# Kernel tuning notes

Measured on AMD Instinct MI355X. Metric: run time of the kernel, lower is better.

The kernel has to match this reference:

```python
import jax, jax.numpy as jnp
import numpy as np

B, NQ, C = 2, 10000, 256
M, L, K = 8, 3, 4
D = C // M
LEVEL_SHAPES = [(100, 100), (50, 50), (25, 25)]


def setup_inputs() -> dict:
    key = jax.random.key(0)
    ks = jax.random.split(key, 16)
    inp = {
        "query": jax.random.normal(ks[0], (B, NQ, C), jnp.float32),
        "reference_points": jax.random.uniform(ks[1], (B, NQ, 2), jnp.float32),
        "value0": jax.random.normal(ks[2], (B, C) + LEVEL_SHAPES[0], jnp.float32),
        "value1": jax.random.normal(ks[3], (B, C) + LEVEL_SHAPES[1], jnp.float32),
        "value2": jax.random.normal(ks[4], (B, C) + LEVEL_SHAPES[2], jnp.float32),
        "Wv": jax.random.normal(ks[5], (C, C), jnp.float32) * 0.02,
        "bv": jnp.zeros((C,), jnp.float32),
        "Ws": jax.random.normal(ks[6], (M * L * K * 2, C), jnp.float32) * 0.05,
        "bs": jax.random.normal(ks[7], (M * L * K * 2,), jnp.float32),
        "Wa": jax.random.normal(ks[8], (M * L * K, C), jnp.float32) * 0.02,
        "ba": jnp.zeros((M * L * K,), jnp.float32),
        "Wo": jax.random.normal(ks[9], (C, C), jnp.float32) * 0.02,
        "bo": jnp.zeros((C,), jnp.float32),
    }
    return inp


def _bilinear_sample(vflat, px, py, H, W):
    """grid_sample bilinear, align_corners=False, padding_mode='zeros'.
    vflat: (B, M, H*W, D); px, py: (B, M, Q, K) pixel coords. -> (B, M, Q, K, D)
    """
    b, m, q, k = px.shape
    x0 = jnp.floor(px)
    y0 = jnp.floor(py)
    wx1 = px - x0  # frac weights (grad 1 w.r.t. px, matching grid_sample)
    wy1 = py - y0
    wx0 = 1.0 - wx1
    wy0 = 1.0 - wy1

    def gather(xi, yi):
        valid = ((xi >= 0) & (xi <= W - 1) & (yi >= 0) & (yi <= H - 1)).astype(vflat.dtype)
        xc = jnp.clip(xi, 0, W - 1).astype(jnp.int32)
        yc = jnp.clip(yi, 0, H - 1).astype(jnp.int32)
        idx = (yc * W + xc).reshape(b, m, q * k)
        g = jnp.take_along_axis(vflat, idx[..., None], axis=2)  # (B,M,QK,D)
        return g.reshape(b, m, q, k, -1) * valid[..., None]

    out = (gather(x0, y0) * (wx0 * wy0)[..., None]
           + gather(x0 + 1, y0) * (wx1 * wy0)[..., None]
           + gather(x0, y0 + 1) * (wx0 * wy1)[..., None]
           + gather(x0 + 1, y0 + 1) * (wx1 * wy1)[..., None])
    return out


def reference(query, reference_points, value0, value1, value2,
              Wv, bv, Ws, bs, Wa, ba, Wo, bo):
    bsz, nq, c = query.shape
    dt = query.dtype
    # sampling offsets and attention weights
    off = (query @ Ws.T + bs).reshape(bsz, nq, M, L, K, 2)
    attn = jax.nn.softmax((query @ Wa.T + ba).reshape(bsz, nq, M, L * K), axis=-1)
    attn = attn.reshape(bsz, nq, M, L, K)

    out = jnp.zeros((bsz, nq, M, D), dt)
    for li, v in enumerate([value0, value1, value2]):
        H, W = v.shape[2], v.shape[3]
        # conv1x1 value projection -> per-head maps (B, M, H*W, D)
        proj = jnp.einsum('bchw,oc->bohw', v, Wv) + bv[None, :, None, None]
        vflat = proj.reshape(bsz, M, D, H * W).transpose(0, 1, 3, 2)
        norm = jnp.asarray([W, H], dt)
        loc = reference_points[:, :, None, None, :] + off[:, :, :, li, :, :] / norm  # (B,Q,M,K,2)
        # grid = loc*2-1; pixel = (grid+1)*size/2 - 0.5 = loc*size - 0.5
        px = (loc[..., 0] * W - 0.5).transpose(0, 2, 1, 3)  # (B,M,Q,K)
        py = (loc[..., 1] * H - 0.5).transpose(0, 2, 1, 3)
        sampled = _bilinear_sample(vflat, px, py, H, W)  # (B,M,Q,K,D)
        out = out + jnp.einsum('bmqkd,bqmk->bqmd', sampled, attn[:, :, :, li, :])

    out = out.reshape(bsz, nq, c)
    return out @ Wo.T + bo
```

## Files before the change

### kernel.cpp

```cpp
#include <hip/hip_runtime.h>
#include <cstddef>

#define B_ 2
#define NQ_ 10000
#define C_ 256
#define M_ 8
#define L_ 3
#define K_ 4
#define D_ 32
#define P_ 13125

typedef unsigned short u16;
typedef __attribute__((ext_vector_type(8))) short short8;
typedef __attribute__((ext_vector_type(4))) float f32x4;

static __device__ __forceinline__ u16 f2bf(float f) {
    union { float f; unsigned u; } x; x.f = f;
    unsigned r = x.u + 0x7fffu + ((x.u >> 16) & 1u);
    return (u16)(r >> 16);
}
static __device__ __forceinline__ short8 cvt8(const float4& a, const float4& b) {
    short8 r;
    r[0] = (short)f2bf(a.x); r[1] = (short)f2bf(a.y);
    r[2] = (short)f2bf(a.z); r[3] = (short)f2bf(a.w);
    r[4] = (short)f2bf(b.x); r[5] = (short)f2bf(b.y);
    r[6] = (short)f2bf(b.z); r[7] = (short)f2bf(b.w);
    return r;
}

__global__ __launch_bounds__(256) void prep(
    const float* __restrict__ v0, const float* __restrict__ v1,
    const float* __restrict__ v2, u16* __restrict__ Vt,
    const float* __restrict__ Wv, const float* __restrict__ Ws,
    const float* __restrict__ Wa, const float* __restrict__ Wo,
    u16* __restrict__ wb,
    const float* __restrict__ query, u16* __restrict__ qbf)
{
    __shared__ u16 tile[64][66];
    const int bid = blockIdx.x;
    const int t   = threadIdx.x;

    if (bid < 3768) {
        constexpr int HWs[3]  = {10000, 2500, 625};
        constexpr int offs[3] = {0, 10000, 12500};
        const int x = bid % 157;
        const int y = (bid / 157) % 4;
        const int z = bid / 628;
        const int b   = z / 3;
        const int lvl = z % 3;
        const int HW  = HWs[lvl];
        const int p0  = x * 64;
        if (p0 >= HW) return;
        const int c0  = y * 64;

        const float* V = (lvl == 0 ? v0 : (lvl == 1 ? v1 : v2)) + (size_t)b * 256 * HW;

        const int pl = t & 63;
        const int cb = t >> 6;
        #pragma unroll
        for (int i = 0; i < 16; ++i) {
            int c = cb + i * 4;
            float vv = 0.f;
            if (p0 + pl < HW)
                vv = V[(size_t)(c0 + c) * HW + p0 + pl];
            tile[pl][c] = f2bf(vv);
        }
        __syncthreads();

        const int cl = t & 63;
        const int pb = t >> 6;
        #pragma unroll
        for (int i = 0; i < 16; ++i) {
            int p = pb + i * 4;
            if (p0 + p < HW)
                Vt[((size_t)b * P_ + offs[lvl] + p0 + p) * 256 + c0 + cl] = tile[p][cl];
        }
    } else if (bid < 3868) {
        const int i = (bid - 3768) * 256 + t;
        if (i >= 25600) return;
        const int g = i * 8;
        const float* src;
        if (g < 65536)       src = Wv + g;
        else if (g < 114688) src = Ws + (g - 65536);
        else if (g < 139264) src = Wa + (g - 114688);
        else                 src = Wo + (g - 139264);
        const float4 a = *reinterpret_cast<const float4*>(src);
        const float4 b = *reinterpret_cast<const float4*>(src + 4);
        *reinterpret_cast<short8*>(wb + g) = cvt8(a, b);
    } else {
        const int i = (bid - 3868) * 256 + t;
        const float4 a = *reinterpret_cast<const float4*>(query + (size_t)i * 8);
        const float4 b = *reinterpret_cast<const float4*>(query + (size_t)i * 8 + 4);
        *reinterpret_cast<short8*>(qbf + (size_t)i * 8) = cvt8(a, b);
    }
}

__global__ __launch_bounds__(512) void gemm_fused(
    const u16* __restrict__ Vt, const u16* __restrict__ qbf,
    const u16* __restrict__ Wvb, const float* __restrict__ bv,
    const u16* __restrict__ Wsb, const float* __restrict__ bs,
    const u16* __restrict__ Wab, const float* __restrict__ ba,
    u16* __restrict__ proj, float* __restrict__ S)
{
    __shared__ u16 Bs[64 * 264];

    const bool jobS = (blockIdx.x >= 416);
    const int  bid  = jobS ? (blockIdx.x - 416) : blockIdx.x;

    const int npanel    = jobS ? 5 : 4;
    const int nRowTiles = jobS ? 79 : 103;
    const int rows      = jobS ? (B_ * NQ_) : (B_ * P_);
    const int N1        = jobS ? 192 : 256;
    const int Ntot      = jobS ? 288 : 256;
    const u16* Aimg     = jobS ? qbf : Vt;
    const u16* B1b      = jobS ? Wsb : Wvb;
    const u16* B2b      = jobS ? Wab : Wvb;
    const float* bias1  = jobS ? bs : bv;
    const float* bias2  = jobS ? ba : bv;

    const int rlo  = bid & 7;
    const int tmp  = bid >> 3;
    const int panel = tmp % npanel;
    const int rowTile = (tmp / npanel) * 8 + rlo;
    if (rowTile >= nRowTiles) return;

    const int t  = threadIdx.x;
    const int w  = t >> 6;
    const int l  = t & 63;
    const int row0 = rowTile * 256 + w * 32;
    const int o0   = panel * 64;
    const int lr = l & 15;
    const int kb = (l >> 4) * 8;

    const int ra0 = min(row0 + lr,      rows - 1);
    const int ra1 = min(row0 + 16 + lr, rows - 1);
    const u16* Ap0 = Aimg + (size_t)ra0 * 256 + kb;
    const u16* Ap1 = Aimg + (size_t)ra1 * 256 + kb;

    short8 A0[4], A1[4];
    #pragma unroll
    for (int i = 0; i < 4; ++i) {
        A0[i] = *reinterpret_cast<const short8*>(Ap0 + i * 32);
        A1[i] = *reinterpret_cast<const short8*>(Ap1 + i * 32);
    }

    #pragma unroll
    for (int i = 0; i < 4; ++i) {
        int idx = i * 512 + t;
        int col = idx >> 5;
        int kc  = (idx & 31) * 8;
        int colg = min(o0 + col, Ntot - 1);
        const u16* Br = ((colg < N1) ? B1b + (size_t)colg * 256
                                     : B2b + (size_t)(colg - N1) * 256) + kc;
        *reinterpret_cast<short8*>(&Bs[col * 264 + kc]) =
            *reinterpret_cast<const short8*>(Br);
    }

    __syncthreads();

    short8 A0b[4], A1b[4];
    #pragma unroll
    for (int i = 0; i < 4; ++i) {
        A0b[i] = *reinterpret_cast<const short8*>(Ap0 + 128 + i * 32);
        A1b[i] = *reinterpret_cast<const short8*>(Ap1 + 128 + i * 32);
    }

    f32x4 acc[2][4] = {};
    #pragma unroll
    for (int i = 0; i < 8; ++i) {
        const int k0 = i * 32;
        short8 a0 = (i < 4) ? A0[i] : A0b[i - 4];
        short8 a1 = (i < 4) ? A1[i] : A1b[i - 4];
        short8 b0 = *reinterpret_cast<const short8*>(&Bs[(0 * 16 + lr) * 264 + kb + k0]);
        short8 b1 = *reinterpret_cast<const short8*>(&Bs[(1 * 16 + lr) * 264 + kb + k0]);
        short8 b2 = *reinterpret_cast<const short8*>(&Bs[(2 * 16 + lr) * 264 + kb + k0]);
        short8 b3 = *reinterpret_cast<const short8*>(&Bs[(3 * 16 + lr) * 264 + kb + k0]);
        acc[0][0] = __builtin_amdgcn_mfma_f32_16x16x32_bf16(a0, b0, acc[0][0], 0, 0, 0);
        acc[0][1] = __builtin_amdgcn_mfma_f32_16x16x32_bf16(a0, b1, acc[0][1], 0, 0, 0);
        acc[0][2] = __builtin_amdgcn_mfma_f32_16x16x32_bf16(a0, b2, acc[0][2], 0, 0, 0);
        acc[0][3] = __builtin_amdgcn_mfma_f32_16x16x32_bf16(a0, b3, acc[0][3], 0, 0, 0);
        acc[1][0] = __builtin_amdgcn_mfma_f32_16x16x32_bf16(a1, b0, acc[1][0], 0, 0, 0);
        acc[1][1] = __builtin_amdgcn_mfma_f32_16x16x32_bf16(a1, b1, acc[1][1], 0, 0, 0);
        acc[1][2] = __builtin_amdgcn_mfma_f32_16x16x32_bf16(a1, b2, acc[1][2], 0, 0, 0);
        acc[1][3] = __builtin_amdgcn_mfma_f32_16x16x32_bf16(a1, b3, acc[1][3], 0, 0, 0);
    }

    const int orow = (l >> 4) * 4;

    if (jobS) {
        #pragma unroll
        for (int ct = 0; ct < 4; ++ct) {
            const int col = o0 + ct * 16 + lr;
            if (col >= Ntot) continue;
            const float bsv = (col < N1) ? bias1[col] : bias2[col - N1];
            #pragma unroll
            for (int rt = 0; rt < 2; ++rt) {
                #pragma unroll
                for (int r = 0; r < 4; ++r) {
                    const int row = row0 + rt * 16 + orow + r;
                    if (row < rows)
                        S[(size_t)row * 288 + col] = acc[rt][ct][r] + bsv;
                }
            }
        }
    } else {
        __syncthreads();
        #pragma unroll
        for (int ct = 0; ct < 4; ++ct) {
            const int col = ct * 16 + lr;
            const float bsv = bias1[o0 + col];
            #pragma unroll
            for (int rt = 0; rt < 2; ++rt) {
                #pragma unroll
                for (int r = 0; r < 4; ++r) {
                    const int rowL = w * 32 + rt * 16 + orow + r;
                    Bs[rowL * 64 + col] = f2bf(acc[rt][ct][r] + bsv);
                }
            }
        }
        __syncthreads();
        const int rowL = t >> 1;
        const int half = (t & 1) * 32;
        const int grow = rowTile * 256 + rowL;
        if (grow < rows) {
            const short8* src = reinterpret_cast<const short8*>(&Bs[rowL * 64 + half]);
            short8* dst = reinterpret_cast<short8*>(proj + (size_t)grow * 256 + o0 + half);
            dst[0] = src[0]; dst[1] = src[1];
            dst[2] = src[2]; dst[3] = src[3];
        }
    }
}

__global__ __launch_bounds__(512) void gemm_out(
    const u16* __restrict__ Av, int rows, int nRowTiles, int npanel,
    const u16* __restrict__ Bb, const float* __restrict__ bias, int Ntot,
    float* __restrict__ Cout)
{
    __shared__ u16 Bs[64 * 264];

    const int bid  = blockIdx.x;
    const int rlo  = bid & 7;
    const int tmp  = bid >> 3;
    const int panel = tmp % npanel;
    const int rowTile = (tmp / npanel) * 8 + rlo;
    if (rowTile >= nRowTiles) return;

    const int t  = threadIdx.x;
    const int w  = t >> 6;
    const int l  = t & 63;
    const int row0 = rowTile * 256 + w * 32;
    const int o0   = panel * 64;
    const int lr = l & 15;
    const int kb = (l >> 4) * 8;

    const int ra0 = min(row0 + lr,      rows - 1);
    const int ra1 = min(row0 + 16 + lr, rows - 1);
    const u16* Ap0 = Av + (size_t)ra0 * 256 + kb;
    const u16* Ap1 = Av + (size_t)ra1 * 256 + kb;

    short8 A0[4], A1[4];
    #pragma unroll
    for (int i = 0; i < 4; ++i) {
        A0[i] = *reinterpret_cast<const short8*>(Ap0 + i * 32);
        A1[i] = *reinterpret_cast<const short8*>(Ap1 + i * 32);
    }

    #pragma unroll
    for (int i = 0; i < 4; ++i) {
        int idx = i * 512 + t;
        int col = idx >> 5;
        int kc  = (idx & 31) * 8;
        int colg = min(o0 + col, Ntot - 1);
        *reinterpret_cast<short8*>(&Bs[col * 264 + kc]) =
            *reinterpret_cast<const short8*>(Bb + (size_t)colg * 256 + kc);
    }

    __syncthreads();

    short8 A0b[4], A1b[4];
    #pragma unroll
    for (int i = 0; i < 4; ++i) {
        A0b[i] = *reinterpret_cast<const short8*>(Ap0 + 128 + i * 32);
        A1b[i] = *reinterpret_cast<const short8*>(Ap1 + 128 + i * 32);
    }

    f32x4 acc[2][4] = {};
    #pragma unroll
    for (int i = 0; i < 8; ++i) {
        const int k0 = i * 32;
        short8 a0 = (i < 4) ? A0[i] : A0b[i - 4];
        short8 a1 = (i < 4) ? A1[i] : A1b[i - 4];
        short8 b0 = *reinterpret_cast<const short8*>(&Bs[(0 * 16 + lr) * 264 + kb + k0]);
        short8 b1 = *reinterpret_cast<const short8*>(&Bs[(1 * 16 + lr) * 264 + kb + k0]);
        short8 b2 = *reinterpret_cast<const short8*>(&Bs[(2 * 16 + lr) * 264 + kb + k0]);
        short8 b3 = *reinterpret_cast<const short8*>(&Bs[(3 * 16 + lr) * 264 + kb + k0]);
        acc[0][0] = __builtin_amdgcn_mfma_f32_16x16x32_bf16(a0, b0, acc[0][0], 0, 0, 0);
        acc[0][1] = __builtin_amdgcn_mfma_f32_16x16x32_bf16(a0, b1, acc[0][1], 0, 0, 0);
        acc[0][2] = __builtin_amdgcn_mfma_f32_16x16x32_bf16(a0, b2, acc[0][2], 0, 0, 0);
        acc[0][3] = __builtin_amdgcn_mfma_f32_16x16x32_bf16(a0, b3, acc[0][3], 0, 0, 0);
        acc[1][0] = __builtin_amdgcn_mfma_f32_16x16x32_bf16(a1, b0, acc[1][0], 0, 0, 0);
        acc[1][1] = __builtin_amdgcn_mfma_f32_16x16x32_bf16(a1, b1, acc[1][1], 0, 0, 0);
        acc[1][2] = __builtin_amdgcn_mfma_f32_16x16x32_bf16(a1, b2, acc[1][2], 0, 0, 0);
        acc[1][3] = __builtin_amdgcn_mfma_f32_16x16x32_bf16(a1, b3, acc[1][3], 0, 0, 0);
    }

    const int orow = (l >> 4) * 4;
    #pragma unroll
    for (int ct = 0; ct < 4; ++ct) {
        const int col = o0 + ct * 16 + lr;
        if (col >= Ntot) continue;
        const float bsv = bias[col];
        #pragma unroll
        for (int rt = 0; rt < 2; ++rt) {
            #pragma unroll
            for (int r = 0; r < 4; ++r) {
                const int row = row0 + rt * 16 + orow + r;
                if (row < rows)
                    Cout[(size_t)row * Ntot + col] = acc[rt][ct][r] + bsv;
            }
        }
    }
}

__global__ __launch_bounds__(256) void sample_kernel(
    const float* __restrict__ S,
    const float* __restrict__ refp,
    const u16* __restrict__ proj,
    u16* __restrict__ out2)
{
    constexpr int Wd[3]   = {100, 50, 25};
    constexpr int offs[3] = {0, 10000, 12500};

    __shared__ int   midx[192][4];
    __shared__ float mw[192][4];

    const int t = threadIdx.x;

    if (t < 192) {
        const int q  = t / 96;
        const int tq = t % 96;
        const int tm = tq / 12;
        const int tj = tq % 12;
        const int bq = blockIdx.x * 2 + q;
        const float* Sq = S + (size_t)bq * 288;

        float lg[12], mx = -1e30f;
        #pragma unroll
        for (int jj = 0; jj < 12; ++jj) {
            lg[jj] = Sq[192 + tm * 12 + jj];
            mx = fmaxf(mx, lg[jj]);
        }
        float sum = 0.f;
        #pragma unroll
        for (int jj = 0; jj < 12; ++jj) sum += __expf(lg[jj] - mx);
        const float attn = __expf(lg[tj] - mx) / sum;

        const int l  = tj >> 2;
        const int Wl = Wd[l];
        const float refx = refp[(size_t)bq * 2 + 0];
        const float refy = refp[(size_t)bq * 2 + 1];
        const float ox = Sq[(tm * 12 + tj) * 2 + 0];
        const float oy = Sq[(tm * 12 + tj) * 2 + 1];
        const float px = refx * (float)Wl + ox - 0.5f;
        const float py = refy * (float)Wl + oy - 0.5f;
        const float x0f = floorf(px), y0f = floorf(py);
        const float wx1 = px - x0f, wy1 = py - y0f;
        const float wx0 = 1.f - wx1, wy0 = 1.f - wy1;
        const int x0 = (int)x0f, y0 = (int)y0f;
        const int x1 = x0 + 1, y1 = y0 + 1;
        const bool vx0 = (unsigned)x0 < (unsigned)Wl;
        const bool vx1 = (unsigned)x1 < (unsigned)Wl;
        const bool vy0 = (unsigned)y0 < (unsigned)Wl;
        const bool vy1 = (unsigned)y1 < (unsigned)Wl;
        const int chb  = tm * 32;
        const int base = offs[l];
        midx[t][0] = (vx0 && vy0) ? ((base + y0 * Wl + x0) * 256 + chb) : 0;
        midx[t][1] = (vx1 && vy0) ? ((base + y0 * Wl + x1) * 256 + chb) : 0;
        midx[t][2] = (vx0 && vy1) ? ((base + y1 * Wl + x0) * 256 + chb) : 0;
        midx[t][3] = (vx1 && vy1) ? ((base + y1 * Wl + x1) * 256 + chb) : 0;
        mw[t][0] = (vx0 && vy0) ? attn * wx0 * wy0 : 0.f;
        mw[t][1] = (vx1 && vy0) ? attn * wx1 * wy0 : 0.f;
        mw[t][2] = (vx0 && vy1) ? attn * wx0 * wy1 : 0.f;
        mw[t][3] = (vx1 && vy1) ? attn * wx1 * wy1 : 0.f;
    }
    __syncthreads();

    const int qi  = t >> 7;
    const int tt  = t & 127;
    const int mh  = tt >> 4;
    const int d16 = tt & 15;
    const int bq2 = blockIdx.x * 2 + qi;
    const int b   = bq2 / NQ_;
    const u16* projb = proj + (size_t)b * P_ * 256 + 2 * d16;

    float acc0 = 0.f, acc1 = 0.f;

    #pragma unroll
    for (int j = 0; j < 12; ++j) {
        const int mj = qi * 96 + mh * 12 + j;
        const int4   o  = *reinterpret_cast<const int4*>(midx[mj]);
        const float4 ww = *reinterpret_cast<const float4*>(mw[mj]);
        const unsigned u00 = *reinterpret_cast<const unsigned*>(projb + o.x);
        const unsigned u10 = *reinterpret_cast<const unsigned*>(projb + o.y);
        const unsigned u01 = *reinterpret_cast<const unsigned*>(projb + o.z);
        const unsigned u11 = *reinterpret_cast<const unsigned*>(projb + o.w);
        union { unsigned u; float f; } c0, c1;
        c0.u = u00 << 16;          c1.u = u00 & 0xffff0000u;
        acc0 = fmaf(ww.x, c0.f, acc0); acc1 = fmaf(ww.x, c1.f, acc1);
        c0.u = u10 << 16;          c1.u = u10 & 0xffff0000u;
        acc0 = fmaf(ww.y, c0.f, acc0); acc1 = fmaf(ww.y, c1.f, acc1);
        c0.u = u01 << 16;          c1.u = u01 & 0xffff0000u;
        acc0 = fmaf(ww.z, c0.f, acc0); acc1 = fmaf(ww.z, c1.f, acc1);
        c0.u = u11 << 16;          c1.u = u11 & 0xffff0000u;
        acc0 = fmaf(ww.w, c0.f, acc0); acc1 = fmaf(ww.w, c1.f, acc1);
    }

    const unsigned packed = (unsigned)f2bf(acc0) | ((unsigned)f2bf(acc1) << 16);
    *reinterpret_cast<unsigned*>(out2 + (size_t)bq2 * 256 + mh * 32 + 2 * d16) = packed;
}

extern "C" void kernel_launch(void* const* d_in, const int* in_sizes, int n_in,
                              void* d_out, int out_size, void* d_ws, size_t ws_size,
                              hipStream_t stream)
{
    const float* query = (const float*)d_in[0];
    const float* refp  = (const float*)d_in[1];
    const float* v0    = (const float*)d_in[2];
    const float* v1    = (const float*)d_in[3];
    const float* v2    = (const float*)d_in[4];
    const float* Wv    = (const float*)d_in[5];
    const float* bv    = (const float*)d_in[6];
    const float* Ws    = (const float*)d_in[7];
    const float* bs    = (const float*)d_in[8];
    const float* Wa    = (const float*)d_in[9];
    const float* ba    = (const float*)d_in[10];
    const float* Wo    = (const float*)d_in[11];
    const float* bo    = (const float*)d_in[12];
    float* out = (float*)d_out;

    char* wsb = (char*)d_ws;
    u16*   proj  = (u16*)wsb;    wsb += (size_t)B_ * P_ * 256 * 2;
    float* S     = (float*)wsb;  wsb += (size_t)B_ * NQ_ * 288 * 4;
    u16*   Vt    = (u16*)wsb;    wsb += (size_t)B_ * P_ * 256 * 2;
    u16*   out2  = (u16*)wsb;    wsb += (size_t)B_ * NQ_ * 256 * 2;
    u16*   qbf   = (u16*)wsb;    wsb += (size_t)B_ * NQ_ * 256 * 2;
    u16*   wb    = (u16*)wsb;    wsb += (size_t)204800 * 2;
    u16* Wvb = wb;
    u16* Wsb = wb + 65536;
    u16* Wab = wb + 114688;
    u16* Wob = wb + 139264;

    prep<<<dim3(6368), dim3(256), 0, stream>>>(
        v0, v1, v2, Vt, Wv, Ws, Wa, Wo, wb, query, qbf);

    gemm_fused<<<dim3(816), dim3(512), 0, stream>>>(
        Vt, qbf, Wvb, bv, Wsb, bs, Wab, ba, proj, S);

    sample_kernel<<<dim3(NQ_), dim3(256), 0, stream>>>(S, refp, proj, out2);

    gemm_out<<<dim3(320), dim3(512), 0, stream>>>(
        out2, B_ * NQ_, 79, 4, Wob, bo, 256, out);
}
```

Measured before the change: 193.1 us.

## Reschedule kernels so value transpose overlaps the offset/attention GEMM

Splits the old prep kernel into a small weight/query bf16 conversion kernel. The value-map transpose moves into a combined kernel with the query-side offset/attention GEMM, so the two independent jobs share one launch. The value projection GEMM becomes its own kernel that runs after the transpose. This adds a fifth launch and an extra dependency step, in exchange for better packing of independent work across CUs.

```diff
diff --git a/kernel.cpp b/kernel.cpp
--- a/kernel.cpp
+++ b/kernel.cpp
@@ -28,55 +28,16 @@
     return r;
 }
 
-__global__ __launch_bounds__(256) void prep(
-    const float* __restrict__ v0, const float* __restrict__ v1,
-    const float* __restrict__ v2, u16* __restrict__ Vt,
+__global__ __launch_bounds__(256) void cvt_wq(
     const float* __restrict__ Wv, const float* __restrict__ Ws,
     const float* __restrict__ Wa, const float* __restrict__ Wo,
     u16* __restrict__ wb,
     const float* __restrict__ query, u16* __restrict__ qbf)
 {
-    __shared__ u16 tile[64][66];
     const int bid = blockIdx.x;
     const int t   = threadIdx.x;
-
-    if (bid < 3768) {
-        constexpr int HWs[3]  = {10000, 2500, 625};
-        constexpr int offs[3] = {0, 10000, 12500};
-        const int x = bid % 157;
-        const int y = (bid / 157) % 4;
-        const int z = bid / 628;
-        const int b   = z / 3;
-        const int lvl = z % 3;
-        const int HW  = HWs[lvl];
-        const int p0  = x * 64;
-        if (p0 >= HW) return;
-        const int c0  = y * 64;
-
-        const float* V = (lvl == 0 ? v0 : (lvl == 1 ? v1 : v2)) + (size_t)b * 256 * HW;
-
-        const int pl = t & 63;
-        const int cb = t >> 6;
-        #pragma unroll
-        for (int i = 0; i < 16; ++i) {
-            int c = cb + i * 4;
-            float vv = 0.f;
-            if (p0 + pl < HW)
-                vv = V[(size_t)(c0 + c) * HW + p0 + pl];
-            tile[pl][c] = f2bf(vv);
-        }
-        __syncthreads();
-
-        const int cl = t & 63;
-        const int pb = t >> 6;
-        #pragma unroll
-        for (int i = 0; i < 16; ++i) {
-            int p = pb + i * 4;
-            if (p0 + p < HW)
-                Vt[((size_t)b * P_ + offs[lvl] + p0 + p) * 256 + c0 + cl] = tile[p][cl];
-        }
-    } else if (bid < 3868) {
-        const int i = (bid - 3768) * 256 + t;
+    if (bid < 100) {
+        const int i = bid * 256 + t;
         if (i >= 25600) return;
         const int g = i * 8;
         const float* src;
@@ -88,41 +49,169 @@
         const float4 b = *reinterpret_cast<const float4*>(src + 4);
         *reinterpret_cast<short8*>(wb + g) = cvt8(a, b);
     } else {
-        const int i = (bid - 3868) * 256 + t;
+        const int i = (bid - 100) * 256 + t;
         const float4 a = *reinterpret_cast<const float4*>(query + (size_t)i * 8);
         const float4 b = *reinterpret_cast<const float4*>(query + (size_t)i * 8 + 4);
         *reinterpret_cast<short8*>(qbf + (size_t)i * 8) = cvt8(a, b);
     }
 }
 
-__global__ __launch_bounds__(512) void gemm_fused(
-    const u16* __restrict__ Vt, const u16* __restrict__ qbf,
-    const u16* __restrict__ Wvb, const float* __restrict__ bv,
+__global__ __launch_bounds__(512) void trans_s(
+    const float* __restrict__ v0, const float* __restrict__ v1,
+    const float* __restrict__ v2, u16* __restrict__ Vt,
+    const u16* __restrict__ qbf,
     const u16* __restrict__ Wsb, const float* __restrict__ bs,
     const u16* __restrict__ Wab, const float* __restrict__ ba,
-    u16* __restrict__ proj, float* __restrict__ S)
+    float* __restrict__ S)
 {
     __shared__ u16 Bs[64 * 264];
-
-    const bool jobS = (blockIdx.x >= 416);
-    const int  bid  = jobS ? (blockIdx.x - 416) : blockIdx.x;
-
-    const int npanel    = jobS ? 5 : 4;
-    const int nRowTiles = jobS ? 79 : 103;
-    const int rows      = jobS ? (B_ * NQ_) : (B_ * P_);
-    const int N1        = jobS ? 192 : 256;
-    const int Ntot      = jobS ? 288 : 256;
-    const u16* Aimg     = jobS ? qbf : Vt;
-    const u16* B1b      = jobS ? Wsb : Wvb;
-    const u16* B2b      = jobS ? Wab : Wvb;
-    const float* bias1  = jobS ? bs : bv;
-    const float* bias2  = jobS ? ba : bv;
-
+    const int t = threadIdx.x;
+
+    if (blockIdx.x < 400) {
+        const int bid = blockIdx.x;
+        const int rlo  = bid & 7;
+        const int tmp  = bid >> 3;
+        const int panel = tmp % 5;
+        const int rowTile = (tmp / 5) * 8 + rlo;
+        if (rowTile >= 79) return;
+
+        const int rows = B_ * NQ_;
+        const int N1 = 192, Ntot = 288;
+
+        const int w  = t >> 6;
+        const int l  = t & 63;
+        const int row0 = rowTile * 256 + w * 32;
+        const int o0   = panel * 64;
+        const int lr = l & 15;
+        const int kb = (l >> 4) * 8;
+
+        const int ra0 = min(row0 + lr,      rows - 1);
+        const int ra1 = min(row0 + 16 + lr, rows - 1);
+        const u16* Ap0 = qbf + (size_t)ra0 * 256 + kb;
+        const u16* Ap1 = qbf + (size_t)ra1 * 256 + kb;
+
+        short8 A0[4], A1[4];
+        #pragma unroll
+        for (int i = 0; i < 4; ++i) {
+            A0[i] = *reinterpret_cast<const short8*>(Ap0 + i * 32);
+            A1[i] = *reinterpret_cast<const short8*>(Ap1 + i * 32);
+        }
+
+        #pragma unroll
+        for (int i = 0; i < 4; ++i) {
+            int idx = i * 512 + t;
+            int col = idx >> 5;
+            int kc  = (idx & 31) * 8;
+            int colg = min(o0 + col, Ntot - 1);
+            const u16* Br = ((colg < N1) ? Wsb + (size_t)colg * 256
+                                         : Wab + (size_t)(colg - N1) * 256) + kc;
+            *reinterpret_cast<short8*>(&Bs[col * 264 + kc]) =
+                *reinterpret_cast<const short8*>(Br);
+        }
+
+        __syncthreads();
+
+        short8 A0b[4], A1b[4];
+        #pragma unroll
+        for (int i = 0; i < 4; ++i) {
+            A0b[i] = *reinterpret_cast<const short8*>(Ap0 + 128 + i * 32);
+            A1b[i] = *reinterpret_cast<const short8*>(Ap1 + 128 + i * 32);
+        }
+
+        f32x4 acc[2][4] = {};
+        #pragma unroll
+        for (int i = 0; i < 8; ++i) {
+            const int k0 = i * 32;
+            short8 a0 = (i < 4) ? A0[i] : A0b[i - 4];
+            short8 a1 = (i < 4) ? A1[i] : A1b[i - 4];
+            short8 b0 = *reinterpret_cast<const short8*>(&Bs[(0 * 16 + lr) * 264 + kb + k0]);
+            short8 b1 = *reinterpret_cast<const short8*>(&Bs[(1 * 16 + lr) * 264 + kb + k0]);
+            short8 b2 = *reinterpret_cast<const short8*>(&Bs[(2 * 16 + lr) * 264 + kb + k0]);
+            short8 b3 = *reinterpret_cast<const short8*>(&Bs[(3 * 16 + lr) * 264 + kb + k0]);
+            acc[0][0] = __builtin_amdgcn_mfma_f32_16x16x32_bf16(a0, b0, acc[0][0], 0, 0, 0);
+            acc[0][1] = __builtin_amdgcn_mfma_f32_16x16x32_bf16(a0, b1, acc[0][1], 0, 0, 0);
+            acc[0][2] = __builtin_amdgcn_mfma_f32_16x16x32_bf16(a0, b2, acc[0][2], 0, 0, 0);
+            acc[0][3] = __builtin_amdgcn_mfma_f32_16x16x32_bf16(a0, b3, acc[0][3], 0, 0, 0);
+            acc[1][0] = __builtin_amdgcn_mfma_f32_16x16x32_bf16(a1, b0, acc[1][0], 0, 0, 0);
+            acc[1][1] = __builtin_amdgcn_mfma_f32_16x16x32_bf16(a1, b1, acc[1][1], 0, 0, 0);
+            acc[1][2] = __builtin_amdgcn_mfma_f32_16x16x32_bf16(a1, b2, acc[1][2], 0, 0, 0);
+            acc[1][3] = __builtin_amdgcn_mfma_f32_16x16x32_bf16(a1, b3, acc[1][3], 0, 0, 0);
+        }
+
+        const int orow = (l >> 4) * 4;
+        #pragma unroll
+        for (int ct = 0; ct < 4; ++ct) {
+            const int col = o0 + ct * 16 + lr;
+            if (col >= Ntot) continue;
+            const float bsv = (col < N1) ? bs[col] : ba[col - N1];
+            #pragma unroll
+            for (int rt = 0; rt < 2; ++rt) {
+                #pragma unroll
+                for (int r = 0; r < 4; ++r) {
+                    const int row = row0 + rt * 16 + orow + r;
+                    if (row < rows)
+                        S[(size_t)row * 288 + col] = acc[rt][ct][r] + bsv;
+                }
+            }
+        }
+    } else {
+        constexpr int HWs[3]  = {10000, 2500, 625};
+        constexpr int offs[3] = {0, 10000, 12500};
+        const int tb = blockIdx.x - 400;
+        const int x = tb % 157;
+        const int y = (tb / 157) % 2;
+        const int z = tb / 314;
+        const int b   = z / 3;
+        const int lvl = z % 3;
+        const int HW  = HWs[lvl];
+        const int p0  = x * 64;
+        if (p0 >= HW) return;
+
+        u16 (*tile)[64][66] = reinterpret_cast<u16 (*)[64][66]>(Bs);
+        const int cc = t >> 8;
+        const int tt = t & 255;
+        const int c0 = y * 128 + cc * 64;
+
+        const float* V = (lvl == 0 ? v0 : (lvl == 1 ? v1 : v2)) + (size_t)b * 256 * HW;
+
+        const int pl = tt & 63;
+        const int cb = tt >> 6;
+        #pragma unroll
+        for (int i = 0; i < 16; ++i) {
+            int c = cb + i * 4;
+            float vv = 0.f;
+            if (p0 + pl < HW)
+                vv = V[(size_t)(c0 + c) * HW + p0 + pl];
+            tile[cc][pl][c] = f2bf(vv);
+        }
+        __syncthreads();
+
+        const int cl = tt & 63;
+        const int pb = tt >> 6;
+        #pragma unroll
+        for (int i = 0; i < 16; ++i) {
+            int p = pb + i * 4;
+            if (p0 + p < HW)
+                Vt[((size_t)b * P_ + offs[lvl] + p0 + p) * 256 + c0 + cl] = tile[cc][p][cl];
+        }
+    }
+}
+
+__global__ __launch_bounds__(512) void gemm_proj(
+    const u16* __restrict__ Vt,
+    const u16* __restrict__ Wvb, const float* __restrict__ bv,
+    u16* __restrict__ proj)
+{
+    __shared__ u16 Bs[64 * 264];
+
+    const int bid = blockIdx.x;
     const int rlo  = bid & 7;
     const int tmp  = bid >> 3;
-    const int panel = tmp % npanel;
-    const int rowTile = (tmp / npanel) * 8 + rlo;
-    if (rowTile >= nRowTiles) return;
+    const int panel = tmp % 4;
+    const int rowTile = (tmp / 4) * 8 + rlo;
+    if (rowTile >= 103) return;
+
+    const int rows = B_ * P_;
 
     const int t  = threadIdx.x;
     const int w  = t >> 6;
@@ -134,8 +223,8 @@
 
     const int ra0 = min(row0 + lr,      rows - 1);
     const int ra1 = min(row0 + 16 + lr, rows - 1);
-    const u16* Ap0 = Aimg + (size_t)ra0 * 256 + kb;
-    const u16* Ap1 = Aimg + (size_t)ra1 * 256 + kb;
+    const u16* Ap0 = Vt + (size_t)ra0 * 256 + kb;
+    const u16* Ap1 = Vt + (size_t)ra1 * 256 + kb;
 
     short8 A0[4], A1[4];
     #pragma unroll
@@ -149,11 +238,8 @@
         int idx = i * 512 + t;
         int col = idx >> 5;
         int kc  = (idx & 31) * 8;
-        int colg = min(o0 + col, Ntot - 1);
-        const u16* Br = ((colg < N1) ? B1b + (size_t)colg * 256
-                                     : B2b + (size_t)(colg - N1) * 256) + kc;
         *reinterpret_cast<short8*>(&Bs[col * 264 + kc]) =
-            *reinterpret_cast<const short8*>(Br);
+            *reinterpret_cast<const short8*>(Wvb + (size_t)(o0 + col) * 256 + kc);
     }
 
     __syncthreads();
@@ -186,48 +272,29 @@
     }
 
     const int orow = (l >> 4) * 4;
-
-    if (jobS) {
-        #pragma unroll
-        for (int ct = 0; ct < 4; ++ct) {
-            const int col = o0 + ct * 16 + lr;
-            if (col >= Ntot) continue;
-            const float bsv = (col < N1) ? bias1[col] : bias2[col - N1];
+    __syncthreads();
+    #pragma unroll
+    for (int ct = 0; ct < 4; ++ct) {
+        const int col = ct * 16 + lr;
+        const float bsv = bv[o0 + col];
+        #pragma unroll
+        for (int rt = 0; rt < 2; ++rt) {
             #pragma unroll
-            for (int rt = 0; rt < 2; ++rt) {
-                #pragma unroll
-                for (int r = 0; r < 4; ++r) {
-                    const int row = row0 + rt * 16 + orow + r;
-                    if (row < rows)
-                        S[(size_t)row * 288 + col] = acc[rt][ct][r] + bsv;
-                }
+            for (int r = 0; r < 4; ++r) {
+                const int rowL = w * 32 + rt * 16 + orow + r;
+                Bs[rowL * 64 + col] = f2bf(acc[rt][ct][r] + bsv);
             }
         }
-    } else {
-        __syncthreads();
-        #pragma unroll
-        for (int ct = 0; ct < 4; ++ct) {
-            const int col = ct * 16 + lr;
-            const float bsv = bias1[o0 + col];
-            #pragma unroll
-            for (int rt = 0; rt < 2; ++rt) {
-                #pragma unroll
-                for (int r = 0; r < 4; ++r) {
-                    const int rowL = w * 32 + rt * 16 + orow + r;
-                    Bs[rowL * 64 + col] = f2bf(acc[rt][ct][r] + bsv);
-                }
-            }
-        }
-        __syncthreads();
-        const int rowL = t >> 1;
-        const int half = (t & 1) * 32;
-        const int grow = rowTile * 256 + rowL;
-        if (grow < rows) {
-            const short8* src = reinterpret_cast<const short8*>(&Bs[rowL * 64 + half]);
-            short8* dst = reinterpret_cast<short8*>(proj + (size_t)grow * 256 + o0 + half);
-            dst[0] = src[0]; dst[1] = src[1];
-            dst[2] = src[2]; dst[3] = src[3];
-        }
+    }
+    __syncthreads();
+    const int rowL = t >> 1;
+    const int half = (t & 1) * 32;
+    const int grow = rowTile * 256 + rowL;
+    if (grow < rows) {
+        const short8* src = reinterpret_cast<const short8*>(&Bs[rowL * 64 + half]);
+        short8* dst = reinterpret_cast<short8*>(proj + (size_t)grow * 256 + o0 + half);
+        dst[0] = src[0]; dst[1] = src[1];
+        dst[2] = src[2]; dst[3] = src[3];
     }
 }
 
@@ -450,11 +517,12 @@
     u16* Wab = wb + 114688;
     u16* Wob = wb + 139264;
 
-    prep<<<dim3(6368), dim3(256), 0, stream>>>(
-        v0, v1, v2, Vt, Wv, Ws, Wa, Wo, wb, query, qbf);
-
-    gemm_fused<<<dim3(816), dim3(512), 0, stream>>>(
-        Vt, qbf, Wvb, bv, Wsb, bs, Wab, ba, proj, S);
+    cvt_wq<<<dim3(2600), dim3(256), 0, stream>>>(Wv, Ws, Wa, Wo, wb, query, qbf);
+
+    trans_s<<<dim3(2284), dim3(512), 0, stream>>>(
+        v0, v1, v2, Vt, qbf, Wsb, bs, Wab, ba, S);
+
+    gemm_proj<<<dim3(416), dim3(512), 0, stream>>>(Vt, Wvb, bv, proj);
 
     sample_kernel<<<dim3(NQ_), dim3(256), 0, stream>>>(S, refp, proj, out2);
 
```

New measurement: 205.0 us. 6.2% more time.
